# Performance work log

Measured on AMD Instinct MI355X. Metric: run time of the kernel, lower is better.

Reference implementation:

```python
import jax, jax.numpy as jnp
import numpy as np

T, N = 64, 512
DL, DA, DV = 300, 128, 128
HL, HA, HV = 256, 128, 128
MEM, DF = 256, 128
H_ATT1, H_ATT2, H_G1, H_G2, H_OUT = 512, 512, 512, 512, 256
BETA, M_MOD = 2.0, 3
ATT_IN = (HL + HA + HV) * 2      # cStar dim (windowsize=2)
G_IN = ATT_IN + MEM


def setup_inputs() -> dict:
    key = jax.random.key(0)
    ks = iter(jax.random.split(key, 48))

    def p(*shape):
        return jax.random.normal(next(ks), shape, jnp.float32) * 0.05

    inp = {}
    inp["x"] = jax.random.normal(next(ks), (T, N, DL + DA + DV), jnp.float32)
    for m, (d, h) in (("l", (DL, HL)), ("a", (DA, HA)), ("v", (DV, HV))):
        inp["Wih_" + m] = p(4 * h, d)   # torch LSTMCell weight_ih [4h, d]
        inp["Whh_" + m] = p(4 * h, h)
        inp["bih_" + m] = p(4 * h)
        inp["bhh_" + m] = p(4 * h)
    inp["att1_w1"], inp["att1_b1"] = p(H_ATT1, ATT_IN), p(H_ATT1)
    inp["att1_w2"], inp["att1_b2"] = p(ATT_IN, H_ATT1), p(ATT_IN)
    inp["att2_w1"], inp["att2_b1"] = p(H_ATT2, ATT_IN), p(H_ATT2)
    inp["att2_w2"], inp["att2_b2"] = p(MEM, H_ATT2), p(MEM)
    inp["g1_w1"], inp["g1_b1"] = p(H_G1, G_IN), p(H_G1)
    inp["g1_w2"], inp["g1_b2"] = p(MEM, H_G1), p(MEM)
    inp["g2_w1"], inp["g2_b1"] = p(H_G2, G_IN), p(H_G2)
    inp["g2_w2"], inp["g2_b2"] = p(MEM, H_G2), p(MEM)
    inp["fl_w"], inp["fl_b"] = p(DF, HL), p(DF)
    inp["fa_w"], inp["fa_b"] = p(DF, HA), p(DF)
    inp["fv_w"], inp["fv_b"] = p(DF, HV), p(DF)
    inp["o_w1"], inp["o_b1"] = p(H_OUT, DF + MEM), p(H_OUT)
    inp["o_w2"], inp["o_b2"] = p(1, H_OUT), p(1)
    return inp


def _lin(z, w, b):
    return z @ w.T + b


def _lstm_cell(xt, h, c, Wih, Whh, bih, bhh):
    # torch.nn.LSTMCell: gate order i, f, g, o
    gates = xt @ Wih.T + h @ Whh.T + bih + bhh
    i, f, g, o = jnp.split(gates, 4, axis=1)
    c2 = jax.nn.sigmoid(f) * c + jax.nn.sigmoid(i) * jnp.tanh(g)
    h2 = jax.nn.sigmoid(o) * jnp.tanh(c2)
    return h2, c2


def reference(x, Wih_l, Whh_l, bih_l, bhh_l, Wih_a, Whh_a, bih_a, bhh_a,
              Wih_v, Whh_v, bih_v, bhh_v,
              att1_w1, att1_b1, att1_w2, att1_b2,
              att2_w1, att2_b1, att2_w2, att2_b2,
              g1_w1, g1_b1, g1_w2, g1_b2, g2_w1, g2_b1, g2_w2, g2_b2,
              fl_w, fl_b, fa_w, fa_b, fv_w, fv_b,
              o_w1, o_b1, o_w2, o_b2):
    n = x.shape[1]

    def step(carry, xt):
        h_l, c_l, h_a, c_a, h_v, c_v, mem = carry
        x_l, x_a, x_v = xt[:, :DL], xt[:, DL:DL + DA], xt[:, DL + DA:]
        nh_l, nc_l = _lstm_cell(x_l, h_l, c_l, Wih_l, Whh_l, bih_l, bhh_l)
        nh_a, nc_a = _lstm_cell(x_a, h_a, c_a, Wih_a, Whh_a, bih_a, bhh_a)
        nh_v, nc_v = _lstm_cell(x_v, h_v, c_v, Wih_v, Whh_v, bih_v, bhh_v)
        # cStar = [prev cells, new cells]  -> [n, ATT_IN]
        cStar = jnp.concatenate([c_l, c_a, c_v, nc_l, nc_a, nc_v], axis=1)
        att = jax.nn.softmax(
            _lin(jax.nn.relu(_lin(cStar, att1_w1, att1_b1)), att1_w2, att1_b2),
            axis=1)
        attended = att * cStar
        cHat = jnp.tanh(
            _lin(jax.nn.relu(_lin(attended, att2_w1, att2_b1)), att2_w2, att2_b2))
        both = jnp.concatenate([attended, mem], axis=1)
        gamma1 = jax.nn.sigmoid(
            _lin(jax.nn.relu(_lin(both, g1_w1, g1_b1)), g1_w2, g1_b2))
        gamma2 = jax.nn.sigmoid(
            _lin(jax.nn.relu(_lin(both, g2_w1, g2_b1)), g2_w2, g2_b2))
        mem = gamma1 * mem + gamma2 * cHat
        return (nh_l, nc_l, nh_a, nc_a, nh_v, nc_v, mem), None

    z = lambda d: jnp.zeros((n, d), x.dtype)
    init = (z(HL), z(HL), z(HA), z(HA), z(HV), z(HV), z(MEM))
    (h_l, c_l, h_a, c_a, h_v, c_v, mem), _ = jax.lax.scan(step, init, x)

    def compute_exp(logits):
        return jnp.exp(logits - jnp.max(logits))  # global max, as in source

    p_l = compute_exp(_lin(h_l, fl_w, fl_b))
    p_a = compute_exp(_lin(h_a, fa_w, fa_b))
    p_v = compute_exp(_lin(h_v, fv_w, fv_b))
    e = BETA / (M_MOD - 1)
    lav = (p_l ** e) * jnp.log(p_l) + (p_a ** e) * jnp.log(p_a) + (p_v ** e) * jnp.log(p_v)
    last_hs = jnp.concatenate([lav, mem], axis=1)
    out = _lin(jax.nn.relu(_lin(last_hs, o_w1, o_b1)), o_w2, o_b2)
    return out.flatten()
```

## Files before the change

### kernel.cpp

```cpp
#include <hip/hip_runtime.h>
#include <string.h>

typedef __bf16 bf16_t;
typedef bf16_t bf16x8 __attribute__((ext_vector_type(8)));
typedef bf16_t bf16x4 __attribute__((ext_vector_type(4)));
typedef float  f32x4  __attribute__((ext_vector_type(4)));

#define MFMA16(a,b,c) __builtin_amdgcn_mfma_f32_16x16x32_bf16((a),(b),(c),0,0,0)

#define TSTEPS 64
#define NB     512
#define DIN    556
#define LDSK   40
#define GRIDP  256
#define GXD    33

#define HWREG_XCC_ID (20 | (0 << 6) | ((4 - 1) << 11))

#define OFF_WIHP_L 0u
#define OFF_WHH_L  327680u
#define OFF_WIHP_A 589824u
#define OFF_WHH_A  655360u
#define OFF_WIHP_V 720896u
#define OFF_WHH_V  786432u
#define OFF_ATT1W1 851968u
#define OFF_ATT1W2 1376256u
#define OFF_ATT2W1 1900544u
#define OFF_ATT2W2 2424832u
#define OFF_G1W1   2555904u
#define OFF_G1W2   3211264u
#define OFF_G2W1   3342336u
#define OFF_G2W2   3997696u
#define OFF_FLW    4128768u
#define OFF_FAW    4161536u
#define OFF_FVW    4177920u

__device__ __forceinline__ float sigmoidf_(float x) {
  return 1.0f / (1.0f + __expf(-x));
}
__device__ __forceinline__ float tanhf_(float x) {
  x = fminf(fmaxf(x, -15.0f), 15.0f);
  float e = __expf(2.0f * x);
  return (e - 1.0f) / (e + 1.0f);
}

struct PArgs {
  const float* x;
  const float* bih_l; const float* bhh_l;
  const float* bih_a; const float* bhh_a;
  const float* bih_v; const float* bhh_v;
  const float* att1_b1; const float* att1_b2;
  const float* att2_b1; const float* att2_b2;
  const float* g1_b1; const float* g1_b2;
  const float* g2_b1; const float* g2_b2;
  const float* fl_b; const float* fa_b; const float* fv_b;
  const float* o_w1; const float* o_b1; const float* o_w2; const float* o_b2;
  const float* cvt_src[17];
  unsigned cvt_dst[17];
  int cvt_K[17]; int cvt_Kpad[17]; int cvt_rows[17];
  bf16_t* POOL; bf16_t* XL; bf16_t* XA; bf16_t* XV;
  bf16_t* HB0; bf16_t* HB1; float* CBUF; float* MEMF; bf16_t* MEMBF;
  bf16_t* CSTAR; bf16_t* Z1; float* LOGB; bf16_t* ATTD; bf16_t* Z3;
  float* PL; float* MAXP; float* BSUM;
  unsigned* BAR;
  float* out;
};


__device__ __forceinline__ void gbar(unsigned* bar, unsigned k, int bid) {
  __syncthreads();
  if (threadIdx.x == 0) {
    __threadfence();
    unsigned* gc   = bar + (bid & 7) * 16;
    unsigned* root = bar + 128;
    if (__hip_atomic_fetch_add(gc, 1u, __ATOMIC_ACQ_REL, __HIP_MEMORY_SCOPE_AGENT)
        == 32u * (k + 1u) - 1u) {
      __hip_atomic_fetch_add(root, 1u, __ATOMIC_ACQ_REL, __HIP_MEMORY_SCOPE_AGENT);
    }
    while (__hip_atomic_load(root, __ATOMIC_RELAXED, __HIP_MEMORY_SCOPE_AGENT)
           < 8u * (k + 1u)) {
      __builtin_amdgcn_s_sleep(1);
    }
    __threadfence();
  }
  __syncthreads();
}

__device__ __forceinline__ void lbar(unsigned* ctr, unsigned target) {
  asm volatile("s_waitcnt vmcnt(0)" ::: "memory");
  __syncthreads();
  if (threadIdx.x == 0) {
    __hip_atomic_fetch_add(ctr, 1u, __ATOMIC_RELAXED, __HIP_MEMORY_SCOPE_AGENT);
    while (__hip_atomic_load(ctr, __ATOMIC_RELAXED, __HIP_MEMORY_SCOPE_AGENT)
           < target) {
      __builtin_amdgcn_s_sleep(1);
    }
    asm volatile("buffer_inv\n\ts_waitcnt vmcnt(0)" ::: "memory");
  }
  __syncthreads();
}

__device__ __forceinline__ void gates_body(const PArgs& p, int job, int t, char* SM) {
  bf16_t* Al = (bf16_t*)SM;
  bf16_t* Wl = (bf16_t*)(SM + 5120);
  float (*Gx)[64][GXD] = (float (*)[64][GXD])(SM + 15360);

  const int tid = threadIdx.x;
  const int m0 = (job >> 4) * 64;
  const int y  = job & 15;

  const bf16_t* hin = (t & 1) ? p.HB1 : p.HB0;
  bf16_t* hout      = (t & 1) ? p.HB0 : p.HB1;

  const bf16_t *xp, *Wih, *Whh;
  int Kx, Hm, hoff, j0, oldbase, boff;
  if (y < 8) {
    xp = p.XL + (size_t)t * NB * 320; Wih = p.POOL + OFF_WIHP_L; Whh = p.POOL + OFF_WHH_L;
    Kx = 320; Hm = 256; hoff = 0; j0 = y * 32; oldbase = 0; boff = 0;
  } else if (y < 12) {
    xp = p.XA + (size_t)t * NB * 128; Wih = p.POOL + OFF_WIHP_A; Whh = p.POOL + OFF_WHH_A;
    Kx = 128; Hm = 128; hoff = 131072; j0 = (y - 8) * 32; oldbase = 256; boff = 1024;
  } else {
    xp = p.XV + (size_t)t * NB * 128; Wih = p.POOL + OFF_WIHP_V; Whh = p.POOL + OFF_WHH_V;
    Kx = 128; Hm = 128; hoff = 196608; j0 = (y - 12) * 32; oldbase = 384; boff = 1536;
  }

  const int wave = tid >> 6, lane = tid & 63;
  const int lrow = lane & 15, quad = lane >> 4;
  const int srow = tid >> 2, schunk = (tid & 3) * 8;
  const int wrow = tid >> 1, wchunk = (tid & 1) * 16;

  f32x4 acc[4][2];
  #pragma unroll
  for (int mi = 0; mi < 4; mi++)
    #pragma unroll
    for (int ni = 0; ni < 2; ni++) acc[mi][ni] = f32x4{0.f, 0.f, 0.f, 0.f};

  const int g = wrow >> 5, jr = wrow & 31;

  for (int ph = 0; ph < 2; ph++) {
    const bf16_t* Ab; const bf16_t* Wb; int lda_, ldw_, K_;
    if (ph == 0) { Ab = xp;           lda_ = Kx; K_ = Kx; Wb = Wih; ldw_ = Kx; }
    else         { Ab = hin + hoff;   lda_ = Hm; K_ = Hm; Wb = Whh; ldw_ = Hm; }

    const bf16_t* Arow = Ab + (size_t)(m0 + srow) * lda_ + schunk;
    const bf16_t* Wrow = Wb + (size_t)(g * Hm + j0 + jr) * ldw_ + wchunk;
    bf16x8 av  = *(const bf16x8*)(Arow);
    bf16x8 wv0 = *(const bf16x8*)(Wrow);
    bf16x8 wv1 = *(const bf16x8*)(Wrow + 8);

    for (int k0 = 0; k0 < K_; k0 += 32) {
      *(bf16x8*)(Al + srow * LDSK + schunk) = av;
      *(bf16x8*)(Wl + wrow * LDSK + wchunk) = wv0;
      *(bf16x8*)(Wl + wrow * LDSK + wchunk + 8) = wv1;
      __syncthreads();
      if (k0 + 32 < K_) {
        av  = *(const bf16x8*)(Arow + k0 + 32);
        wv0 = *(const bf16x8*)(Wrow + k0 + 32);
        wv1 = *(const bf16x8*)(Wrow + k0 + 40);
      }
      bf16x8 afr[4], bfr[2];
      #pragma unroll
      for (int mi = 0; mi < 4; mi++)
        afr[mi] = *(const bf16x8*)(Al + (mi * 16 + lrow) * LDSK + quad * 8);
      #pragma unroll
      for (int ni = 0; ni < 2; ni++)
        bfr[ni] = *(const bf16x8*)(Wl + (wave * 32 + ni * 16 + lrow) * LDSK + quad * 8);
      #pragma unroll
      for (int mi = 0; mi < 4; mi++)
        #pragma unroll
        for (int ni = 0; ni < 2; ni++)
          acc[mi][ni] = MFMA16(afr[mi], bfr[ni], acc[mi][ni]);
      __syncthreads();
    }
  }

  #pragma unroll
  for (int mi = 0; mi < 4; mi++)
    #pragma unroll
    for (int ni = 0; ni < 2; ni++) {
      int col = ni * 16 + lrow;
      float bv = p.BSUM[boff + wave * Hm + j0 + col];
      #pragma unroll
      for (int r = 0; r < 4; r++) {
        Gx[wave][mi * 16 + quad * 4 + r][col] = acc[mi][ni][r] + bv;
      }
    }
  __syncthreads();

  float* cbuf = p.CBUF + hoff;
  int m = tid >> 2, jb = (tid & 3) * 8;
  #pragma unroll
  for (int i = 0; i < 8; i++) {
    int j = jb + i;
    float gi = Gx[0][m][j], gf = Gx[1][m][j], gg = Gx[2][m][j], go = Gx[3][m][j];
    size_t off = (size_t)(m0 + m) * Hm + (j0 + j);
    float c_old = cbuf[off];
    float c2 = sigmoidf_(gf) * c_old + sigmoidf_(gi) * tanhf_(gg);
    float h2 = sigmoidf_(go) * tanhf_(c2);
    cbuf[off] = c2;
    hout[hoff + off] = (bf16_t)h2;
    size_t cs = (size_t)(m0 + m) * 1024 + oldbase + (j0 + j);
    p.CSTAR[cs] = (bf16_t)c_old;
    p.CSTAR[cs + 512] = (bf16_t)c2;
  }
  __syncthreads();
}

__device__ __forceinline__ void lin_body(
    const bf16_t* __restrict__ A, int lda,
    const bf16_t* __restrict__ W, int ldw,
    const float* __restrict__ bias,
    bf16_t* Cb, float* Cf, int ldc, int K, int act,
    int m0, int n0, char* SM)
{
  bf16_t* Al = (bf16_t*)SM;
  bf16_t* Wl = (bf16_t*)(SM + 5120);
  const int tid = threadIdx.x;
  const int wave = tid >> 6, lane = tid & 63;
  const int wm = (wave >> 1) * 32, wn = (wave & 1) * 32;
  const int lrow = lane & 15, quad = lane >> 4;
  const int srow = tid >> 2, schunk = (tid & 3) * 8;

  f32x4 acc[2][2];
  #pragma unroll
  for (int mi = 0; mi < 2; mi++)
    #pragma unroll
    for (int ni = 0; ni < 2; ni++) acc[mi][ni] = f32x4{0.f, 0.f, 0.f, 0.f};

  const bf16_t* Arow = A + (size_t)(m0 + srow) * lda + schunk;
  const bf16_t* Wrow = W + (size_t)(n0 + srow) * ldw + schunk;
  bf16x8 av = *(const bf16x8*)(Arow);
  bf16x8 wv = *(const bf16x8*)(Wrow);

  for (int k0 = 0; k0 < K; k0 += 32) {
    *(bf16x8*)(Al + srow * LDSK + schunk) = av;
    *(bf16x8*)(Wl + srow * LDSK + schunk) = wv;
    __syncthreads();
    if (k0 + 32 < K) {
      av = *(const bf16x8*)(Arow + k0 + 32);
      wv = *(const bf16x8*)(Wrow + k0 + 32);
    }
    bf16x8 a0 = *(const bf16x8*)(Al + (wm + lrow) * LDSK + quad * 8);
    bf16x8 a1 = *(const bf16x8*)(Al + (wm + 16 + lrow) * LDSK + quad * 8);
    bf16x8 b0 = *(const bf16x8*)(Wl + (wn + lrow) * LDSK + quad * 8);
    bf16x8 b1 = *(const bf16x8*)(Wl + (wn + 16 + lrow) * LDSK + quad * 8);
    acc[0][0] = MFMA16(a0, b0, acc[0][0]);
    acc[0][1] = MFMA16(a0, b1, acc[0][1]);
    acc[1][0] = MFMA16(a1, b0, acc[1][0]);
    acc[1][1] = MFMA16(a1, b1, acc[1][1]);
    __syncthreads();
  }
  #pragma unroll
  for (int mi = 0; mi < 2; mi++)
    #pragma unroll
    for (int ni = 0; ni < 2; ni++) {
      int row0 = m0 + wm + mi * 16 + quad * 4;
      int col = n0 + wn + ni * 16 + lrow;
      float bv = bias[col];
      #pragma unroll
      for (int r = 0; r < 4; r++) {
        float v = acc[mi][ni][r] + bv;
        if (act == 1) v = fmaxf(v, 0.f);
        size_t off = (size_t)(row0 + r) * ldc + col;
        if (Cb) Cb[off] = (bf16_t)v;
        if (Cf) Cf[off] = v;
      }
    }
}

__device__ __forceinline__ void softmax_body(const PArgs& p, int n, char* SM) {
  float* red = (float*)SM;
  const int tid = threadIdx.x;
  float4 v = *(const float4*)(p.LOGB + (size_t)n * 1024 + tid * 4);
  float mx = fmaxf(fmaxf(v.x, v.y), fmaxf(v.z, v.w));
  red[tid] = mx; __syncthreads();
  for (int s = 128; s > 0; s >>= 1) {
    if (tid < s) red[tid] = fmaxf(red[tid], red[tid + s]);
    __syncthreads();
  }
  mx = red[0]; __syncthreads();
  float e0 = __expf(v.x - mx), e1 = __expf(v.y - mx);
  float e2 = __expf(v.z - mx), e3 = __expf(v.w - mx);
  red[tid] = e0 + e1 + e2 + e3; __syncthreads();
  for (int s = 128; s > 0; s >>= 1) {
    if (tid < s) red[tid] += red[tid + s];
    __syncthreads();
  }
  float inv = 1.0f / red[0];
  bf16x4 c4 = *(const bf16x4*)(p.CSTAR + (size_t)n * 1024 + tid * 4);
  bf16x4 o;
  o[0] = (bf16_t)(e0 * inv * (float)c4[0]);
  o[1] = (bf16_t)(e1 * inv * (float)c4[1]);
  o[2] = (bf16_t)(e2 * inv * (float)c4[2]);
  o[3] = (bf16_t)(e3 * inv * (float)c4[3]);
  *(bf16x4*)(p.ATTD + (size_t)n * 1024 + tid * 4) = o;
  __syncthreads();
}

__device__ __forceinline__ void z3_body(const PArgs& p, int job, char* SM) {
  bf16_t* Al = (bf16_t*)SM;
  bf16_t* Wl = (bf16_t*)(SM + 5120);
  const int tid = threadIdx.x;
  const int m0 = (job & 7) * 64, n0 = (job >> 3) * 64;
  const int wave = tid >> 6, lane = tid & 63;
  const int wm = (wave >> 1) * 32, wn = (wave & 1) * 32;
  const int lrow = lane & 15, quad = lane >> 4;
  const int srow = tid >> 2, schunk = (tid & 3) * 8;

  const bf16_t* W; const float* b; int K, nloc;
  if (n0 < 512)       { W = p.POOL + OFF_ATT2W1; b = p.att2_b1; K = 1024; nloc = n0; }
  else if (n0 < 1024) { W = p.POOL + OFF_G1W1;  b = p.g1_b1;  K = 1280; nloc = n0 - 512; }
  else                { W = p.POOL + OFF_G2W1;  b = p.g2_b1;  K = 1280; nloc = n0 - 1024; }

  f32x4 acc[2][2];
  #pragma unroll
  for (int mi = 0; mi < 2; mi++)
    #pragma unroll
    for (int ni = 0; ni < 2; ni++) acc[mi][ni] = f32x4{0.f, 0.f, 0.f, 0.f};

  const bf16_t* Aatt = p.ATTD + (size_t)(m0 + srow) * 1024 + schunk;
  const bf16_t* Amem = p.MEMBF + (size_t)(m0 + srow) * 256 + schunk;
  const bf16_t* Wrow = W + (size_t)(nloc + srow) * K + schunk;
  bf16x8 av = *(const bf16x8*)(Aatt);
  bf16x8 wv = *(const bf16x8*)(Wrow);

  for (int k0 = 0; k0 < K; k0 += 32) {
    *(bf16x8*)(Al + srow * LDSK + schunk) = av;
    *(bf16x8*)(Wl + srow * LDSK + schunk) = wv;
    __syncthreads();
    int kn = k0 + 32;
    if (kn < K) {
      av = (kn < 1024) ? *(const bf16x8*)(Aatt + kn)
                       : *(const bf16x8*)(Amem + (kn - 1024));
      wv = *(const bf16x8*)(Wrow + kn);
    }
    bf16x8 a0 = *(const bf16x8*)(Al + (wm + lrow) * LDSK + quad * 8);
    bf16x8 a1 = *(const bf16x8*)(Al + (wm + 16 + lrow) * LDSK + quad * 8);
    bf16x8 b0 = *(const bf16x8*)(Wl + (wn + lrow) * LDSK + quad * 8);
    bf16x8 b1 = *(const bf16x8*)(Wl + (wn + 16 + lrow) * LDSK + quad * 8);
    acc[0][0] = MFMA16(a0, b0, acc[0][0]);
    acc[0][1] = MFMA16(a0, b1, acc[0][1]);
    acc[1][0] = MFMA16(a1, b0, acc[1][0]);
    acc[1][1] = MFMA16(a1, b1, acc[1][1]);
    __syncthreads();
  }
  #pragma unroll
  for (int mi = 0; mi < 2; mi++)
    #pragma unroll
    for (int ni = 0; ni < 2; ni++) {
      int row0 = m0 + wm + mi * 16 + quad * 4;
      int cloc = wn + ni * 16 + lrow;
      float bv = b[nloc + cloc];
      #pragma unroll
      for (int r = 0; r < 4; r++) {
        float v = fmaxf(acc[mi][ni][r] + bv, 0.f);
        p.Z3[(size_t)(row0 + r) * 1536 + n0 + cloc] = (bf16_t)v;
      }
    }
}

__device__ __forceinline__ void gmem_body(const PArgs& p, int job, char* SM) {
  const int tid = threadIdx.x;
  const int m0 = (job & 7) * 64, n0 = (job >> 3) * 64;
  const int wave = tid >> 6, lane = tid & 63;
  const int wm = (wave >> 1) * 32, wn = (wave & 1) * 32;
  const int lrow = lane & 15, quad = lane >> 4;
  const int srow = tid >> 2, schunk = (tid & 3) * 8;

  const bf16_t* Ws[3] = { p.POOL + OFF_ATT2W2, p.POOL + OFF_G1W2, p.POOL + OFF_G2W2 };

  f32x4 acc[3][2][2];
  #pragma unroll
  for (int s = 0; s < 3; s++)
    #pragma unroll
    for (int mi = 0; mi < 2; mi++)
      #pragma unroll
      for (int ni = 0; ni < 2; ni++) acc[s][mi][ni] = f32x4{0.f, 0.f, 0.f, 0.f};

  const bf16_t* Arow = p.Z3 + (size_t)(m0 + srow) * 1536 + schunk;
  bf16x8 avv[3], wvv[3];
  #pragma unroll
  for (int s = 0; s < 3; s++) {
    avv[s] = *(const bf16x8*)(Arow + s * 512);
    wvv[s] = *(const bf16x8*)(Ws[s] + (size_t)(n0 + srow) * 512 + schunk);
  }

  for (int k0 = 0; k0 < 512; k0 += 32) {
    #pragma unroll
    for (int s = 0; s < 3; s++) {
      bf16_t* Az = (bf16_t*)(SM + s * 5120);
      bf16_t* Wz = (bf16_t*)(SM + 15360 + s * 5120);
      *(bf16x8*)(Az + srow * LDSK + schunk) = avv[s];
      *(bf16x8*)(Wz + srow * LDSK + schunk) = wvv[s];
    }
    __syncthreads();
    if (k0 + 32 < 512) {
      #pragma unroll
      for (int s = 0; s < 3; s++) {
// ... 47 lines not shown
  }
  red[tid] = mx; __syncthreads();
  for (int s = 128; s > 0; s >>= 1) {
    if (tid < s) red[tid] = fmaxf(red[tid], red[tid + s]);
    __syncthreads();
  }
  if (tid == 0) p.MAXP[job] = red[0];
  __syncthreads();
}

__device__ __forceinline__ void out_body(const PArgs& p, int n, char* SM) {
  float* hs  = (float*)SM;
  float* red = (float*)(SM + 1536);
  float* Ms  = (float*)(SM + 2560);
  const int tid = threadIdx.x;
  if (tid < 3) {
    float m = -3.4e38f;
    #pragma unroll
    for (int i = 0; i < 16; i++) m = fmaxf(m, p.MAXP[tid * 16 + i]);
    Ms[tid] = m;
  }
  __syncthreads();
  const float M0 = Ms[0], M1 = Ms[1], M2 = Ms[2];
  for (int idx = tid; idx < 384; idx += 256) {
    float v;
    if (idx < 128) {
      float d0 = p.PL[(size_t)n * 384 + idx] - M0;
      float d1 = p.PL[(size_t)n * 384 + 128 + idx] - M1;
      float d2 = p.PL[(size_t)n * 384 + 256 + idx] - M2;
      v = __expf(d0) * d0 + __expf(d1) * d1 + __expf(d2) * d2;
    } else {
      v = p.MEMF[(size_t)n * 256 + idx - 128];
    }
    hs[idx] = v;
  }
  __syncthreads();
  float acc = p.o_b1[tid];
  const float* wr = p.o_w1 + (size_t)tid * 384;
  #pragma unroll 4
  for (int k = 0; k < 384; k += 4) {
    float4 w = *(const float4*)(wr + k);
    acc += w.x * hs[k] + w.y * hs[k + 1] + w.z * hs[k + 2] + w.w * hs[k + 3];
  }
  red[tid] = fmaxf(acc, 0.f) * p.o_w2[tid];
  __syncthreads();
  for (int s = 128; s > 0; s >>= 1) {
    if (tid < s) red[tid] += red[tid + s];
    __syncthreads();
  }
  if (tid == 0) p.out[n] = red[0] + p.o_b2[0];
  __syncthreads();
}

__global__ void __launch_bounds__(256) persist_kernel(PArgs p) {
  __shared__ __align__(16) char SM[49152];
  __shared__ int meta[12];
  const int bid = blockIdx.x;
  const int tid = threadIdx.x;
  unsigned bk = 0;

  {
    float4* z = (float4*)p.HB0;
    for (int i = bid * 256 + tid; i < 180224; i += GRIDP * 256)
      z[i] = make_float4(0.f, 0.f, 0.f, 0.f);

    int gid = bid * 256 + tid;
    if (gid < 1024)      p.BSUM[gid] = p.bih_l[gid] + p.bhh_l[gid];
    else if (gid < 1536) p.BSUM[gid] = p.bih_a[gid - 1024] + p.bhh_a[gid - 1024];
    else if (gid < 2048) p.BSUM[gid] = p.bih_v[gid - 1536] + p.bhh_v[gid - 1536];

    for (int r = bid; r < TSTEPS * NB; r += GRIDP) {
      const float4* xr = (const float4*)(p.x + (size_t)r * DIN);
      int q = tid;
      if (q < 144) {
        float4 v; bf16_t* dst;
        if (q < 80) {
          v = (q < 75) ? xr[q] : make_float4(0.f, 0.f, 0.f, 0.f);
          dst = p.XL + (size_t)r * 320 + q * 4;
        } else if (q < 112) {
          v = xr[75 + (q - 80)];
          dst = p.XA + (size_t)r * 128 + (q - 80) * 4;
        } else {
          v = xr[107 + (q - 112)];
          dst = p.XV + (size_t)r * 128 + (q - 112) * 4;
        }
        bf16x4 o;
        o[0] = (bf16_t)v.x; o[1] = (bf16_t)v.y; o[2] = (bf16_t)v.z; o[3] = (bf16_t)v.w;
        *(bf16x4*)dst = o;
      }
    }

    for (int m = 0; m < 17; m++) {
      const float* src = p.cvt_src[m];
      bf16_t* dst = p.POOL + p.cvt_dst[m];
      int K = p.cvt_K[m], Kp = p.cvt_Kpad[m], R = p.cvt_rows[m];
      int Kq = Kp >> 2, Ksq = K >> 2;
      for (int r = bid; r < R; r += GRIDP) {
        const float4* sr = (const float4*)(src + (size_t)r * K);
        for (int q = tid; q < Kq; q += 256) {
          float4 v = (q < Ksq) ? sr[q] : make_float4(0.f, 0.f, 0.f, 0.f);
          bf16x4 o;
          o[0] = (bf16_t)v.x; o[1] = (bf16_t)v.y; o[2] = (bf16_t)v.z; o[3] = (bf16_t)v.w;
          *(bf16x4*)(dst + (size_t)r * Kp + q * 4) = o;
        }
      }
    }

    if (tid == 0) {
      unsigned raw = __builtin_amdgcn_s_getreg(HWREG_XCC_ID);
      if (raw > 7u) {
        __hip_atomic_store(p.BAR + 159, 1u, __ATOMIC_RELAXED, __HIP_MEMORY_SCOPE_AGENT);
        raw &= 7u;
      }
      meta[0] = (int)raw;
      meta[1] = (int)__hip_atomic_fetch_add(p.BAR + 160 + raw * 16, 1u,
                    __ATOMIC_RELAXED, __HIP_MEMORY_SCOPE_AGENT);
    }
  }
  gbar(p.BAR, bk++, bid);

  if (tid < 8)
    meta[2 + tid] = (int)__hip_atomic_load(p.BAR + 160 + tid * 16,
                        __ATOMIC_RELAXED, __HIP_MEMORY_SCOPE_AGENT);
  if (tid == 8)
    meta[10] = (int)__hip_atomic_load(p.BAR + 159,
                   __ATOMIC_RELAXED, __HIP_MEMORY_SCOPE_AGENT);
  __syncthreads();
  int total = 0; bool localmode = (meta[10] == 0);
  #pragma unroll
  for (int i = 0; i < 8; i++) {
    total += meta[2 + i];
    if (meta[2 + i] == 0) localmode = false;
  }
  if (total != GRIDP) localmode = false;

  if (localmode) {
    const int g = meta[0];
    const int rank = meta[1];
    const unsigned cnt = (unsigned)meta[2 + g];
    unsigned* lctr = p.BAR + 288 + g * 16;
    unsigned lk = 0;

    for (int t = 0; t < TSTEPS; t++) {
      for (int j = rank; j < 16; j += (int)cnt) gates_body(p, g * 16 + j, t, SM);
      lbar(lctr, cnt * (++lk));

      for (int j = rank; j < 8; j += (int)cnt)
        lin_body(p.CSTAR, 1024, p.POOL + OFF_ATT1W1, 1024, p.att1_b1,
                 p.Z1, (float*)0, 512, 1024, 1, g * 64, j * 64, SM);
      lbar(lctr, cnt * (++lk));

      for (int j = rank; j < 16; j += (int)cnt)
        lin_body(p.Z1, 512, p.POOL + OFF_ATT1W2, 512, p.att1_b2,
                 (bf16_t*)0, p.LOGB, 1024, 512, 0, g * 64, j * 64, SM);
      lbar(lctr, cnt * (++lk));

      for (int j = rank; j < 64; j += (int)cnt) softmax_body(p, g * 64 + j, SM);
      lbar(lctr, cnt * (++lk));

      for (int j = rank; j < 24; j += (int)cnt) z3_body(p, (j << 3) | g, SM);
      lbar(lctr, cnt * (++lk));

      for (int j = rank; j < 4; j += (int)cnt) gmem_body(p, (j << 3) | g, SM);
    }
  } else {
    for (int t = 0; t < TSTEPS; t++) {
      for (int job = bid; job < 128; job += GRIDP) gates_body(p, job, t, SM);
      gbar(p.BAR, bk++, bid);

      for (int job = bid; job < 64; job += GRIDP)
        lin_body(p.CSTAR, 1024, p.POOL + OFF_ATT1W1, 1024, p.att1_b1,
                 p.Z1, (float*)0, 512, 1024, 1, (job & 7) * 64, (job >> 3) * 64, SM);
      gbar(p.BAR, bk++, bid);

      for (int job = bid; job < 128; job += GRIDP)
        lin_body(p.Z1, 512, p.POOL + OFF_ATT1W2, 512, p.att1_b2,
                 (bf16_t*)0, p.LOGB, 1024, 512, 0, (job & 7) * 64, (job >> 3) * 64, SM);
      gbar(p.BAR, bk++, bid);

      for (int job = bid; job < 512; job += GRIDP) softmax_body(p, job, SM);
      gbar(p.BAR, bk++, bid);

      for (int job = bid; job < 192; job += GRIDP) z3_body(p, job, SM);
      gbar(p.BAR, bk++, bid);

      for (int job = bid; job < 32; job += GRIDP) gmem_body(p, job, SM);
    }
  }
  gbar(p.BAR, bk++, bid);

  for (int job = bid; job < 48; job += GRIDP) {
    int mat = job >> 4, rem = job & 15;
    int m0 = (rem & 7) * 64, n0 = (rem >> 3) * 64;
    const bf16_t* h = (mat == 0) ? p.HB0 : (mat == 1) ? p.HB0 + 131072 : p.HB0 + 196608;
    int lda = (mat == 0) ? 256 : 128;
    const bf16_t* W = p.POOL + ((mat == 0) ? OFF_FLW : (mat == 1) ? OFF_FAW : OFF_FVW);
    const float* b = (mat == 0) ? p.fl_b : (mat == 1) ? p.fa_b : p.fv_b;
    lin_body(h, lda, W, lda, b, (bf16_t*)0, p.PL + mat * 128, 384, lda, 0, m0, n0, SM);
  }
  gbar(p.BAR, bk++, bid);

  for (int job = bid; job < 48; job += GRIDP) maxpart_body(p, job, SM);
  gbar(p.BAR, bk++, bid);

  for (int job = bid; job < 512; job += GRIDP) out_body(p, job, SM);
}


__global__ __launch_bounds__(256) void zero_kernel(float4* p, int n4) {
  int i = blockIdx.x * 256 + threadIdx.x;
  if (i < n4) p[i] = make_float4(0.f, 0.f, 0.f, 0.f);
}

__global__ __launch_bounds__(256) void cvt_pad_kernel(
    const float* __restrict__ src, bf16_t* __restrict__ dst, int K, int Kpad)
{
  int r = blockIdx.x;
  for (int k = threadIdx.x; k < Kpad; k += 256)
    dst[(size_t)r * Kpad + k] = (k < K) ? (bf16_t)src[(size_t)r * K + k] : (bf16_t)0.f;
}

__global__ __launch_bounds__(256) void cvt_x_kernel(
    const float* __restrict__ x, bf16_t* __restrict__ xl,
    bf16_t* __restrict__ xa, bf16_t* __restrict__ xv)
{
  int r = blockIdx.x;
  const float* xr = x + (size_t)r * DIN;
  for (int c = threadIdx.x; c < 576; c += 256) {
    if (c < 320) {
      xl[(size_t)r * 320 + c] = (c < 300) ? (bf16_t)xr[c] : (bf16_t)0.f;
    } else if (c < 448) {
      xa[(size_t)r * 128 + (c - 320)] = (bf16_t)xr[300 + (c - 320)];
    } else {
      xv[(size_t)r * 128 + (c - 448)] = (bf16_t)xr[428 + (c - 448)];
    }
  }
}

__global__ __launch_bounds__(256) void bias_sum_kernel(
    const float* __restrict__ bih_l, const float* __restrict__ bhh_l,
    const float* __restrict__ bih_a, const float* __restrict__ bhh_a,
    const float* __restrict__ bih_v, const float* __restrict__ bhh_v,
    float* __restrict__ bsum)
{
  int i = blockIdx.x * 256 + threadIdx.x;
  if (i < 1024)      bsum[i] = bih_l[i] + bhh_l[i];
  else if (i < 1536) bsum[i] = bih_a[i - 1024] + bhh_a[i - 1024];
  else if (i < 2048) bsum[i] = bih_v[i - 1536] + bhh_v[i - 1536];
}

__global__ __launch_bounds__(256) void gates_cell_kernel_fb(PArgs p, int t) {
  __shared__ __align__(16) char SM[49152];
  gates_body(p, blockIdx.x * 16 + blockIdx.y, t, SM);
}

__global__ __launch_bounds__(256) void mfma_lin_kernel_fb(
    const bf16_t* A, int lda, const bf16_t* W, int ldw,
    const float* bias, bf16_t* Cb, float* Cf, int ldc, int K, int act)
{
  __shared__ __align__(16) char SM[10240];
  lin_body(A, lda, W, ldw, bias, Cb, Cf, ldc, K, act,
           blockIdx.x * 64, blockIdx.y * 64, SM);
}

__global__ __launch_bounds__(256) void softmax_attend_kernel_fb(PArgs p) {
  __shared__ __align__(16) char SM[1024];
  softmax_body(p, blockIdx.x, SM);
}

__global__ __launch_bounds__(256) void z3_kernel_fb(PArgs p) {
  __shared__ __align__(16) char SM[10240];
  z3_body(p, blockIdx.x + blockIdx.y * 8, SM);
}

__global__ __launch_bounds__(256) void gmem_kernel_fb(PArgs p) {
  __shared__ __align__(16) char SM[30720];
  gmem_body(p, blockIdx.x + blockIdx.y * 8, SM);
}

__global__ __launch_bounds__(256) void maxpart_kernel_fb(PArgs p) {
  __shared__ __align__(16) char SM[1024];
  maxpart_body(p, blockIdx.x, SM);
}

__global__ __launch_bounds__(256) void out_kernel_fb(PArgs p) {
  __shared__ __align__(16) char SM[2576];
  out_body(p, blockIdx.x, SM);
}

extern "C" void kernel_launch(void* const* d_in, const int* in_sizes, int n_in,
                              void* d_out, int out_size, void* d_ws, size_t ws_size,
                              hipStream_t stream)
{
  const float* x      = (const float*)d_in[0];
  const float* Wih_l  = (const float*)d_in[1];
  const float* Whh_l  = (const float*)d_in[2];
  const float* bih_l  = (const float*)d_in[3];
  const float* bhh_l  = (const float*)d_in[4];
  const float* Wih_a  = (const float*)d_in[5];
  const float* Whh_a  = (const float*)d_in[6];
  const float* bih_a  = (const float*)d_in[7];
  const float* bhh_a  = (const float*)d_in[8];
  const float* Wih_v  = (const float*)d_in[9];
  const float* Whh_v  = (const float*)d_in[10];
  const float* bih_v  = (const float*)d_in[11];
  const float* bhh_v  = (const float*)d_in[12];
  const float* att1_w1 = (const float*)d_in[13];
  const float* att1_b1 = (const float*)d_in[14];
  const float* att1_w2 = (const float*)d_in[15];
  const float* att1_b2 = (const float*)d_in[16];
  const float* att2_w1 = (const float*)d_in[17];
  const float* att2_b1 = (const float*)d_in[18];
  const float* att2_w2 = (const float*)d_in[19];
  const float* att2_b2 = (const float*)d_in[20];
  const float* g1_w1  = (const float*)d_in[21];
  const float* g1_b1  = (const float*)d_in[22];
  const float* g1_w2  = (const float*)d_in[23];
  const float* g1_b2  = (const float*)d_in[24];
  const float* g2_w1  = (const float*)d_in[25];
  const float* g2_b1  = (const float*)d_in[26];
  const float* g2_w2  = (const float*)d_in[27];
  const float* g2_b2  = (const float*)d_in[28];
  const float* fl_w   = (const float*)d_in[29];
  const float* fl_b   = (const float*)d_in[30];
  const float* fa_w   = (const float*)d_in[31];
  const float* fa_b   = (const float*)d_in[32];
  const float* fv_w   = (const float*)d_in[33];
  const float* fv_b   = (const float*)d_in[34];
  const float* o_w1   = (const float*)d_in[35];
  const float* o_b1   = (const float*)d_in[36];
  const float* o_w2   = (const float*)d_in[37];
  const float* o_b2   = (const float*)d_in[38];

  char* base = (char*)d_ws;
  PArgs pa;
  pa.x = x;
  pa.bih_l = bih_l; pa.bhh_l = bhh_l;
  pa.bih_a = bih_a; pa.bhh_a = bhh_a;
  pa.bih_v = bih_v; pa.bhh_v = bhh_v;
  pa.att1_b1 = att1_b1; pa.att1_b2 = att1_b2;
  pa.att2_b1 = att2_b1; pa.att2_b2 = att2_b2;
  pa.g1_b1 = g1_b1; pa.g1_b2 = g1_b2;
  pa.g2_b1 = g2_b1; pa.g2_b2 = g2_b2;
  pa.fl_b = fl_b; pa.fa_b = fa_b; pa.fv_b = fv_b;
  pa.o_w1 = o_w1; pa.o_b1 = o_b1; pa.o_w2 = o_w2; pa.o_b2 = o_b2;

  const float* csrc[17] = { Wih_l, Whh_l, Wih_a, Whh_a, Wih_v, Whh_v,
                            att1_w1, att1_w2, att2_w1, att2_w2,
                            g1_w1, g1_w2, g2_w1, g2_w2, fl_w, fa_w, fv_w };
  const unsigned cdst[17] = { OFF_WIHP_L, OFF_WHH_L, OFF_WIHP_A, OFF_WHH_A,
                              OFF_WIHP_V, OFF_WHH_V, OFF_ATT1W1, OFF_ATT1W2,
                              OFF_ATT2W1, OFF_ATT2W2, OFF_G1W1, OFF_G1W2,
                              OFF_G2W1, OFF_G2W2, OFF_FLW, OFF_FAW, OFF_FVW };
  const int cK[17]   = { 300, 256, 128, 128, 128, 128, 1024, 512, 1024, 512,
                         1280, 512, 1280, 512, 256, 128, 128 };
  const int cKp[17]  = { 320, 256, 128, 128, 128, 128, 1024, 512, 1024, 512,
                         1280, 512, 1280, 512, 256, 128, 128 };
  const int cR[17]   = { 1024, 1024, 512, 512, 512, 512, 512, 1024, 512, 256,
                         512, 256, 512, 256, 128, 128, 128 };
  for (int i = 0; i < 17; i++) {
    pa.cvt_src[i] = csrc[i]; pa.cvt_dst[i] = cdst[i];
    pa.cvt_K[i] = cK[i]; pa.cvt_Kpad[i] = cKp[i]; pa.cvt_rows[i] = cR[i];
  }

  pa.POOL  = (bf16_t*)(base);
  pa.XL    = (bf16_t*)(base + 8388608);
  pa.XA    = (bf16_t*)(base + 29360128);
  pa.XV    = (bf16_t*)(base + 37748736);
  pa.HB0   = (bf16_t*)(base + 46137344);
  pa.HB1   = (bf16_t*)(base + 46661632);
  pa.CBUF  = (float*) (base + 47185920);
  pa.MEMF  = (float*) (base + 48234496);
  pa.MEMBF = (bf16_t*)(base + 48758784);
  pa.CSTAR = (bf16_t*)(base + 49020928);
  pa.Z1    = (bf16_t*)(base + 50069504);
  pa.LOGB  = (float*) (base + 50593792);
  pa.ATTD  = (bf16_t*)(base + 52690944);
  pa.Z3    = (bf16_t*)(base + 53739520);
  pa.PL    = (float*) (base + 55312384);
  pa.MAXP  = (float*) (base + 56098816);
  pa.BSUM  = (float*) (base + 56099072);
  pa.BAR   = (unsigned*)(base + 56107264);
  pa.out   = (float*)d_out;

  hipMemsetAsync(pa.BAR, 0, 2048, stream);

  void* kargs[] = { (void*)&pa };
  hipError_t e = hipLaunchCooperativeKernel((const void*)persist_kernel,
                                            dim3(GRIDP), dim3(256), kargs, 0, stream);
  if (e == hipSuccess) return;

  zero_kernel<<<704, 256, 0, stream>>>((float4*)pa.HB0, 180224);
  cvt_x_kernel<<<TSTEPS * NB, 256, 0, stream>>>(x, pa.XL, pa.XA, pa.XV);
  for (int i = 0; i < 17; i++)
    cvt_pad_kernel<<<cR[i], 256, 0, stream>>>(csrc[i], pa.POOL + cdst[i], cK[i], cKp[i]);
  bias_sum_kernel<<<8, 256, 0, stream>>>(bih_l, bhh_l, bih_a, bhh_a, bih_v, bhh_v, pa.BSUM);

  for (int t = 0; t < TSTEPS; t++) {
    gates_cell_kernel_fb<<<dim3(8, 16), 256, 0, stream>>>(pa, t);
    mfma_lin_kernel_fb<<<dim3(8, 8), 256, 0, stream>>>(
        pa.CSTAR, 1024, pa.POOL + OFF_ATT1W1, 1024, att1_b1,
        pa.Z1, (float*)nullptr, 512, 1024, 1);
    mfma_lin_kernel_fb<<<dim3(8, 16), 256, 0, stream>>>(
        pa.Z1, 512, pa.POOL + OFF_ATT1W2, 512, att1_b2,
        (bf16_t*)nullptr, pa.LOGB, 1024, 512, 0);
    softmax_attend_kernel_fb<<<512, 256, 0, stream>>>(pa);
    z3_kernel_fb<<<dim3(8, 24), 256, 0, stream>>>(pa);
    gmem_kernel_fb<<<dim3(8, 4), 256, 0, stream>>>(pa);
  }

  bf16_t* h_l = pa.HB0;
  bf16_t* h_a = pa.HB0 + 131072;
  bf16_t* h_v = pa.HB0 + 196608;
  mfma_lin_kernel_fb<<<dim3(8, 2), 256, 0, stream>>>(
      h_l, 256, pa.POOL + OFF_FLW, 256, fl_b, (bf16_t*)nullptr, pa.PL, 384, 256, 0);
  mfma_lin_kernel_fb<<<dim3(8, 2), 256, 0, stream>>>(
      h_a, 128, pa.POOL + OFF_FAW, 128, fa_b, (bf16_t*)nullptr, pa.PL + 128, 384, 128, 0);
  mfma_lin_kernel_fb<<<dim3(8, 2), 256, 0, stream>>>(
      h_v, 128, pa.POOL + OFF_FVW, 128, fv_b, (bf16_t*)nullptr, pa.PL + 256, 384, 128, 0);
  maxpart_kernel_fb<<<48, 256, 0, stream>>>(pa);
  out_kernel_fb<<<512, 256, 0, stream>>>(pa);
}
```

Measured before the change: 4.829 ms.

## Overlap LSTM gates with previous step's attention chain via team split and double-buffered LDS

Splits each XCC group of 32 blocks into a team of 8 that computes LSTM gates for step t and a team of 24 that runs the attention/memory chain for step t-1. The chain reads a double-buffered cStar (CSTAR/CSTAR2), which makes this possible because the memory update does not feed back into the LSTM. All MFMA GEMM bodies also get double-buffered LDS tiles, so one barrier per k-iteration is removed. This adds a second counter barrier set, enlarges the barrier memset, requires extra workspace (gated by ws_size), and adds a missing gbar in the fallback path.

```diff
diff --git a/kernel.cpp b/kernel.cpp
--- a/kernel.cpp
+++ b/kernel.cpp
@@ -60,10 +60,11 @@
   int cvt_K[17]; int cvt_Kpad[17]; int cvt_rows[17];
   bf16_t* POOL; bf16_t* XL; bf16_t* XA; bf16_t* XV;
   bf16_t* HB0; bf16_t* HB1; float* CBUF; float* MEMF; bf16_t* MEMBF;
-  bf16_t* CSTAR; bf16_t* Z1; float* LOGB; bf16_t* ATTD; bf16_t* Z3;
+  bf16_t* CSTAR; bf16_t* CSTAR2; bf16_t* Z1; float* LOGB; bf16_t* ATTD; bf16_t* Z3;
   float* PL; float* MAXP; float* BSUM;
   unsigned* BAR;
   float* out;
+  int allow_team;
 };
 
 
@@ -100,17 +101,17 @@
   __syncthreads();
 }
 
-__device__ __forceinline__ void gates_body(const PArgs& p, int job, int t, char* SM) {
-  bf16_t* Al = (bf16_t*)SM;
-  bf16_t* Wl = (bf16_t*)(SM + 5120);
-  float (*Gx)[64][GXD] = (float (*)[64][GXD])(SM + 15360);
+__device__ __forceinline__ void gates_body(const PArgs& p, int job, int t, char* SM,
+                                           const bf16_t* hbase, bf16_t* houtb,
+                                           bf16_t* cstar)
+{
+  bf16_t* AlB[2] = { (bf16_t*)SM,            (bf16_t*)(SM + 5120) };
+  bf16_t* WlB[2] = { (bf16_t*)(SM + 10240),  (bf16_t*)(SM + 20480) };
+  float (*Gx)[64][GXD] = (float (*)[64][GXD])SM;
 
   const int tid = threadIdx.x;
   const int m0 = (job >> 4) * 64;
   const int y  = job & 15;
-
-  const bf16_t* hin = (t & 1) ? p.HB1 : p.HB0;
-  bf16_t* hout      = (t & 1) ? p.HB0 : p.HB1;
 
   const bf16_t *xp, *Wih, *Whh;
   int Kx, Hm, hoff, j0, oldbase, boff;
@@ -129,50 +130,58 @@
   const int lrow = lane & 15, quad = lane >> 4;
   const int srow = tid >> 2, schunk = (tid & 3) * 8;
   const int wrow = tid >> 1, wchunk = (tid & 1) * 16;
+  const int g = wrow >> 5, jr = wrow & 31;
 
   f32x4 acc[4][2];
   #pragma unroll
   for (int mi = 0; mi < 4; mi++)
     #pragma unroll
     for (int ni = 0; ni < 2; ni++) acc[mi][ni] = f32x4{0.f, 0.f, 0.f, 0.f};
-
-  const int g = wrow >> 5, jr = wrow & 31;
 
   for (int ph = 0; ph < 2; ph++) {
     const bf16_t* Ab; const bf16_t* Wb; int lda_, ldw_, K_;
-    if (ph == 0) { Ab = xp;           lda_ = Kx; K_ = Kx; Wb = Wih; ldw_ = Kx; }
-    else         { Ab = hin + hoff;   lda_ = Hm; K_ = Hm; Wb = Whh; ldw_ = Hm; }
+    if (ph == 0) { Ab = xp;            lda_ = Kx; K_ = Kx; Wb = Wih; ldw_ = Kx; }
+    else         { Ab = hbase + hoff;  lda_ = Hm; K_ = Hm; Wb = Whh; ldw_ = Hm; }
 
     const bf16_t* Arow = Ab + (size_t)(m0 + srow) * lda_ + schunk;
     const bf16_t* Wrow = Wb + (size_t)(g * Hm + j0 + jr) * ldw_ + wchunk;
+    const int nI = K_ >> 5;
+
     bf16x8 av  = *(const bf16x8*)(Arow);
     bf16x8 wv0 = *(const bf16x8*)(Wrow);
     bf16x8 wv1 = *(const bf16x8*)(Wrow + 8);
-
-    for (int k0 = 0; k0 < K_; k0 += 32) {
-      *(bf16x8*)(Al + srow * LDSK + schunk) = av;
-      *(bf16x8*)(Wl + wrow * LDSK + wchunk) = wv0;
-      *(bf16x8*)(Wl + wrow * LDSK + wchunk + 8) = wv1;
+    *(bf16x8*)(AlB[0] + srow * LDSK + schunk) = av;
+    *(bf16x8*)(WlB[0] + wrow * LDSK + wchunk) = wv0;
+    *(bf16x8*)(WlB[0] + wrow * LDSK + wchunk + 8) = wv1;
+
+    for (int i = 0; i < nI; i++) {
+      const int cur = i & 1;
+      const bool more = (i + 1 < nI);
+      if (more) {
+        av  = *(const bf16x8*)(Arow + (i + 1) * 32);
+        wv0 = *(const bf16x8*)(Wrow + (i + 1) * 32);
+        wv1 = *(const bf16x8*)(Wrow + (i + 1) * 32 + 8);
+      }
       __syncthreads();
-      if (k0 + 32 < K_) {
-        av  = *(const bf16x8*)(Arow + k0 + 32);
-        wv0 = *(const bf16x8*)(Wrow + k0 + 32);
-        wv1 = *(const bf16x8*)(Wrow + k0 + 40);
+      if (more) {
+        *(bf16x8*)(AlB[cur ^ 1] + srow * LDSK + schunk) = av;
+        *(bf16x8*)(WlB[cur ^ 1] + wrow * LDSK + wchunk) = wv0;
+        *(bf16x8*)(WlB[cur ^ 1] + wrow * LDSK + wchunk + 8) = wv1;
       }
       bf16x8 afr[4], bfr[2];
       #pragma unroll
       for (int mi = 0; mi < 4; mi++)
-        afr[mi] = *(const bf16x8*)(Al + (mi * 16 + lrow) * LDSK + quad * 8);
+        afr[mi] = *(const bf16x8*)(AlB[cur] + (mi * 16 + lrow) * LDSK + quad * 8);
       #pragma unroll
       for (int ni = 0; ni < 2; ni++)
-        bfr[ni] = *(const bf16x8*)(Wl + (wave * 32 + ni * 16 + lrow) * LDSK + quad * 8);
+        bfr[ni] = *(const bf16x8*)(WlB[cur] + (wave * 32 + ni * 16 + lrow) * LDSK + quad * 8);
       #pragma unroll
       for (int mi = 0; mi < 4; mi++)
         #pragma unroll
         for (int ni = 0; ni < 2; ni++)
           acc[mi][ni] = MFMA16(afr[mi], bfr[ni], acc[mi][ni]);
-      __syncthreads();
-    }
+    }
+    __syncthreads();
   }
 
   #pragma unroll
@@ -199,10 +208,10 @@
     float c2 = sigmoidf_(gf) * c_old + sigmoidf_(gi) * tanhf_(gg);
     float h2 = sigmoidf_(go) * tanhf_(c2);
     cbuf[off] = c2;
-    hout[hoff + off] = (bf16_t)h2;
+    houtb[hoff + off] = (bf16_t)h2;
     size_t cs = (size_t)(m0 + m) * 1024 + oldbase + (j0 + j);
-    p.CSTAR[cs] = (bf16_t)c_old;
-    p.CSTAR[cs + 512] = (bf16_t)c2;
+    cstar[cs] = (bf16_t)c_old;
+    cstar[cs + 512] = (bf16_t)c2;
   }
   __syncthreads();
 }
@@ -214,8 +223,8 @@
     bf16_t* Cb, float* Cf, int ldc, int K, int act,
     int m0, int n0, char* SM)
 {
-  bf16_t* Al = (bf16_t*)SM;
-  bf16_t* Wl = (bf16_t*)(SM + 5120);
+  bf16_t* AlB[2] = { (bf16_t*)SM,            (bf16_t*)(SM + 5120) };
+  bf16_t* WlB[2] = { (bf16_t*)(SM + 10240),  (bf16_t*)(SM + 15360) };
   const int tid = threadIdx.x;
   const int wave = tid >> 6, lane = tid & 63;
   const int wm = (wave >> 1) * 32, wn = (wave & 1) * 32;
@@ -230,27 +239,36 @@
 
   const bf16_t* Arow = A + (size_t)(m0 + srow) * lda + schunk;
   const bf16_t* Wrow = W + (size_t)(n0 + srow) * ldw + schunk;
+  const int nI = K >> 5;
+
   bf16x8 av = *(const bf16x8*)(Arow);
   bf16x8 wv = *(const bf16x8*)(Wrow);
-
-  for (int k0 = 0; k0 < K; k0 += 32) {
-    *(bf16x8*)(Al + srow * LDSK + schunk) = av;
-    *(bf16x8*)(Wl + srow * LDSK + schunk) = wv;
+  *(bf16x8*)(AlB[0] + srow * LDSK + schunk) = av;
+  *(bf16x8*)(WlB[0] + srow * LDSK + schunk) = wv;
+
+  for (int i = 0; i < nI; i++) {
+    const int cur = i & 1;
+    const bool more = (i + 1 < nI);
+    if (more) {
+      av = *(const bf16x8*)(Arow + (i + 1) * 32);
+      wv = *(const bf16x8*)(Wrow + (i + 1) * 32);
+    }
     __syncthreads();
-    if (k0 + 32 < K) {
-      av = *(const bf16x8*)(Arow + k0 + 32);
-      wv = *(const bf16x8*)(Wrow + k0 + 32);
-    }
-    bf16x8 a0 = *(const bf16x8*)(Al + (wm + lrow) * LDSK + quad * 8);
-    bf16x8 a1 = *(const bf16x8*)(Al + (wm + 16 + lrow) * LDSK + quad * 8);
-    bf16x8 b0 = *(const bf16x8*)(Wl + (wn + lrow) * LDSK + quad * 8);
-    bf16x8 b1 = *(const bf16x8*)(Wl + (wn + 16 + lrow) * LDSK + quad * 8);
+    if (more) {
+      *(bf16x8*)(AlB[cur ^ 1] + srow * LDSK + schunk) = av;
+      *(bf16x8*)(WlB[cur ^ 1] + srow * LDSK + schunk) = wv;
+    }
+    bf16x8 a0 = *(const bf16x8*)(AlB[cur] + (wm + lrow) * LDSK + quad * 8);
+    bf16x8 a1 = *(const bf16x8*)(AlB[cur] + (wm + 16 + lrow) * LDSK + quad * 8);
+    bf16x8 b0 = *(const bf16x8*)(WlB[cur] + (wn + lrow) * LDSK + quad * 8);
+    bf16x8 b1 = *(const bf16x8*)(WlB[cur] + (wn + 16 + lrow) * LDSK + quad * 8);
     acc[0][0] = MFMA16(a0, b0, acc[0][0]);
     acc[0][1] = MFMA16(a0, b1, acc[0][1]);
     acc[1][0] = MFMA16(a1, b0, acc[1][0]);
     acc[1][1] = MFMA16(a1, b1, acc[1][1]);
-    __syncthreads();
-  }
+  }
+  __syncthreads();
+
   #pragma unroll
   for (int mi = 0; mi < 2; mi++)
     #pragma unroll
@@ -269,7 +287,8 @@
     }
 }
 
-__device__ __forceinline__ void softmax_body(const PArgs& p, int n, char* SM) {
+__device__ __forceinline__ void softmax_body(const PArgs& p, int n, char* SM,
+                                             const bf16_t* cstar) {
   float* red = (float*)SM;
   const int tid = threadIdx.x;
   float4 v = *(const float4*)(p.LOGB + (size_t)n * 1024 + tid * 4);
@@ -288,7 +307,7 @@
     __syncthreads();
   }
   float inv = 1.0f / red[0];
-  bf16x4 c4 = *(const bf16x4*)(p.CSTAR + (size_t)n * 1024 + tid * 4);
+  bf16x4 c4 = *(const bf16x4*)(cstar + (size_t)n * 1024 + tid * 4);
   bf16x4 o;
   o[0] = (bf16_t)(e0 * inv * (float)c4[0]);
   o[1] = (bf16_t)(e1 * inv * (float)c4[1]);
@@ -299,8 +318,8 @@
 }
 
 __device__ __forceinline__ void z3_body(const PArgs& p, int job, char* SM) {
-  bf16_t* Al = (bf16_t*)SM;
-  bf16_t* Wl = (bf16_t*)(SM + 5120);
+  bf16_t* AlB[2] = { (bf16_t*)SM,            (bf16_t*)(SM + 5120) };
+  bf16_t* WlB[2] = { (bf16_t*)(SM + 10240),  (bf16_t*)(SM + 15360) };
   const int tid = threadIdx.x;
   const int m0 = (job & 7) * 64, n0 = (job >> 3) * 64;
   const int wave = tid >> 6, lane = tid & 63;
@@ -322,29 +341,38 @@
   const bf16_t* Aatt = p.ATTD + (size_t)(m0 + srow) * 1024 + schunk;
   const bf16_t* Amem = p.MEMBF + (size_t)(m0 + srow) * 256 + schunk;
   const bf16_t* Wrow = W + (size_t)(nloc + srow) * K + schunk;
+  const int nI = K >> 5;
+
   bf16x8 av = *(const bf16x8*)(Aatt);
   bf16x8 wv = *(const bf16x8*)(Wrow);
-
-  for (int k0 = 0; k0 < K; k0 += 32) {
-    *(bf16x8*)(Al + srow * LDSK + schunk) = av;
-    *(bf16x8*)(Wl + srow * LDSK + schunk) = wv;
-    __syncthreads();
-    int kn = k0 + 32;
-    if (kn < K) {
+  *(bf16x8*)(AlB[0] + srow * LDSK + schunk) = av;
+  *(bf16x8*)(WlB[0] + srow * LDSK + schunk) = wv;
+
+  for (int i = 0; i < nI; i++) {
+    const int cur = i & 1;
+    const bool more = (i + 1 < nI);
+    if (more) {
+      int kn = (i + 1) * 32;
       av = (kn < 1024) ? *(const bf16x8*)(Aatt + kn)
                        : *(const bf16x8*)(Amem + (kn - 1024));
       wv = *(const bf16x8*)(Wrow + kn);
     }
-    bf16x8 a0 = *(const bf16x8*)(Al + (wm + lrow) * LDSK + quad * 8);
-    bf16x8 a1 = *(const bf16x8*)(Al + (wm + 16 + lrow) * LDSK + quad * 8);
-    bf16x8 b0 = *(const bf16x8*)(Wl + (wn + lrow) * LDSK + quad * 8);
-    bf16x8 b1 = *(const bf16x8*)(Wl + (wn + 16 + lrow) * LDSK + quad * 8);
+    __syncthreads();
+    if (more) {
+      *(bf16x8*)(AlB[cur ^ 1] + srow * LDSK + schunk) = av;
+      *(bf16x8*)(WlB[cur ^ 1] + srow * LDSK + schunk) = wv;
+    }
+    bf16x8 a0 = *(const bf16x8*)(AlB[cur] + (wm + lrow) * LDSK + quad * 8);
+    bf16x8 a1 = *(const bf16x8*)(AlB[cur] + (wm + 16 + lrow) * LDSK + quad * 8);
+    bf16x8 b0 = *(const bf16x8*)(WlB[cur] + (wn + lrow) * LDSK + quad * 8);
+    bf16x8 b1 = *(const bf16x8*)(WlB[cur] + (wn + 16 + lrow) * LDSK + quad * 8);
     acc[0][0] = MFMA16(a0, b0, acc[0][0]);
     acc[0][1] = MFMA16(a0, b1, acc[0][1]);
     acc[1][0] = MFMA16(a1, b0, acc[1][0]);
     acc[1][1] = MFMA16(a1, b1, acc[1][1]);
-    __syncthreads();
-  }
+  }
+  __syncthreads();
+
   #pragma unroll
   for (int mi = 0; mi < 2; mi++)
     #pragma unroll
@@ -498,8 +526,27 @@
   __syncthreads();
 }
 
+__device__ __forceinline__ void attn_chain(const PArgs& p, int g, int rb,
+                                           const bf16_t* cs_prev, char* SM,
+                                           unsigned* teamc, unsigned& tk)
+{
+  if (rb < 8)
+    lin_body(cs_prev, 1024, p.POOL + OFF_ATT1W1, 1024, p.att1_b1,
+             p.Z1, (float*)0, 512, 1024, 1, g * 64, rb * 64, SM);
+  lbar(teamc, 24u * (++tk));
+  if (rb < 16)
+    lin_body(p.Z1, 512, p.POOL + OFF_ATT1W2, 512, p.att1_b2,
+             (bf16_t*)0, p.LOGB, 1024, 512, 0, g * 64, rb * 64, SM);
+  lbar(teamc, 24u * (++tk));
+  for (int j = rb; j < 64; j += 24) softmax_body(p, g * 64 + j, SM, cs_prev);
+  lbar(teamc, 24u * (++tk));
+  z3_body(p, (rb << 3) | g, SM);
+  lbar(teamc, 24u * (++tk));
+  if (rb < 4) gmem_body(p, (rb << 3) | g, SM);
+}
+
 __global__ void __launch_bounds__(256) persist_kernel(PArgs p) {
-  __shared__ __align__(16) char SM[49152];
+  __shared__ __align__(16) char SM[34816];
   __shared__ int meta[12];
   const int bid = blockIdx.x;
   const int tid = threadIdx.x;
@@ -572,46 +619,41 @@
     meta[10] = (int)__hip_atomic_load(p.BAR + 159,
                    __ATOMIC_RELAXED, __HIP_MEMORY_SCOPE_AGENT);
   __syncthreads();
-  int total = 0; bool localmode = (meta[10] == 0);
-  #pragma unroll
-  for (int i = 0; i < 8; i++) {
-    total += meta[2 + i];
-    if (meta[2 + i] == 0) localmode = false;
-  }
-  if (total != GRIDP) localmode = false;
-
-  if (localmode) {
+  bool teammode = (meta[10] == 0) && (p.allow_team != 0);
+  #pragma unroll
+  for (int i = 0; i < 8; i++)
+    if (meta[2 + i] != 32) teammode = false;
+
+  if (teammode) {
     const int g = meta[0];
     const int rank = meta[1];
-    const unsigned cnt = (unsigned)meta[2 + g];
-    unsigned* lctr = p.BAR + 288 + g * 16;
-    unsigned lk = 0;
+    unsigned* fullc = p.BAR + 288 + g * 16;
+    unsigned* teamc = p.BAR + 416 + g * 16;
+    unsigned lk = 0, tk = 0;
+    const int ra = rank - 24;
+    const int rb = rank;
 
     for (int t = 0; t < TSTEPS; t++) {
-      for (int j = rank; j < 16; j += (int)cnt) gates_body(p, g * 16 + j, t, SM);
-      lbar(lctr, cnt * (++lk));
-
-      for (int j = rank; j < 8; j += (int)cnt)
-        lin_body(p.CSTAR, 1024, p.POOL + OFF_ATT1W1, 1024, p.att1_b1,
-                 p.Z1, (float*)0, 512, 1024, 1, g * 64, j * 64, SM);
-      lbar(lctr, cnt * (++lk));
-
-      for (int j = rank; j < 16; j += (int)cnt)
-        lin_body(p.Z1, 512, p.POOL + OFF_ATT1W2, 512, p.att1_b2,
-                 (bf16_t*)0, p.LOGB, 1024, 512, 0, g * 64, j * 64, SM);
-      lbar(lctr, cnt * (++lk));
-
-      for (int j = rank; j < 64; j += (int)cnt) softmax_body(p, g * 64 + j, SM);
-      lbar(lctr, cnt * (++lk));
-
-      for (int j = rank; j < 24; j += (int)cnt) z3_body(p, (j << 3) | g, SM);
-      lbar(lctr, cnt * (++lk));
-
-      for (int j = rank; j < 4; j += (int)cnt) gmem_body(p, (j << 3) | g, SM);
-    }
+      lbar(fullc, 32u * (++lk));
+      const bf16_t* hin = (t & 1) ? p.HB1 : p.HB0;
+      bf16_t* hout      = (t & 1) ? p.HB0 : p.HB1;
+      bf16_t* cs_cur    = (t & 1) ? p.CSTAR2 : p.CSTAR;
+      const bf16_t* cs_prev = (t & 1) ? p.CSTAR : p.CSTAR2;
+      if (ra >= 0) {
+        gates_body(p, g * 16 + ra,     t, SM, hin, hout, cs_cur);
+        gates_body(p, g * 16 + 8 + ra, t, SM, hin, hout, cs_cur);
+      } else if (t > 0) {
+        attn_chain(p, g, rb, cs_prev, SM, teamc, tk);
+      }
+    }
+    lbar(fullc, 32u * (++lk));
+    if (ra < 0) attn_chain(p, g, rb, p.CSTAR2, SM, teamc, tk);
   } else {
     for (int t = 0; t < TSTEPS; t++) {
-      for (int job = bid; job < 128; job += GRIDP) gates_body(p, job, t, SM);
+      const bf16_t* hin = (t & 1) ? p.HB1 : p.HB0;
+      bf16_t* hout      = (t & 1) ? p.HB0 : p.HB1;
+      for (int job = bid; job < 128; job += GRIDP)
+        gates_body(p, job, t, SM, hin, hout, p.CSTAR);
       gbar(p.BAR, bk++, bid);
 
       for (int job = bid; job < 64; job += GRIDP)
@@ -624,13 +666,15 @@
                  (bf16_t*)0, p.LOGB, 1024, 512, 0, (job & 7) * 64, (job >> 3) * 64, SM);
       gbar(p.BAR, bk++, bid);
 
-      for (int job = bid; job < 512; job += GRIDP) softmax_body(p, job, SM);
+      for (int job = bid; job < 512; job += GRIDP)
+        softmax_body(p, job, SM, p.CSTAR);
       gbar(p.BAR, bk++, bid);
 
       for (int job = bid; job < 192; job += GRIDP) z3_body(p, job, SM);
       gbar(p.BAR, bk++, bid);
 
       for (int job = bid; job < 32; job += GRIDP) gmem_body(p, job, SM);
+      gbar(p.BAR, bk++, bid);
     }
   }
   gbar(p.BAR, bk++, bid);
@@ -696,26 +740,28 @@
 }
 
 __global__ __launch_bounds__(256) void gates_cell_kernel_fb(PArgs p, int t) {
-  __shared__ __align__(16) char SM[49152];
-  gates_body(p, blockIdx.x * 16 + blockIdx.y, t, SM);
+  __shared__ __align__(16) char SM[34816];
+  const bf16_t* hin = (t & 1) ? p.HB1 : p.HB0;
+  bf16_t* hout      = (t & 1) ? p.HB0 : p.HB1;
+  gates_body(p, blockIdx.x * 16 + blockIdx.y, t, SM, hin, hout, p.CSTAR);
 }
 
 __global__ __launch_bounds__(256) void mfma_lin_kernel_fb(
     const bf16_t* A, int lda, const bf16_t* W, int ldw,
     const float* bias, bf16_t* Cb, float* Cf, int ldc, int K, int act)
 {
-  __shared__ __align__(16) char SM[10240];
+  __shared__ __align__(16) char SM[20480];
   lin_body(A, lda, W, ldw, bias, Cb, Cf, ldc, K, act,
            blockIdx.x * 64, blockIdx.y * 64, SM);
 }
 
 __global__ __launch_bounds__(256) void softmax_attend_kernel_fb(PArgs p) {
   __shared__ __align__(16) char SM[1024];
-  softmax_body(p, blockIdx.x, SM);
+  softmax_body(p, blockIdx.x, SM, p.CSTAR);
 }
 
 __global__ __launch_bounds__(256) void z3_kernel_fb(PArgs p) {
-  __shared__ __align__(16) char SM[10240];
+  __shared__ __align__(16) char SM[20480];
   z3_body(p, blockIdx.x + blockIdx.y * 8, SM);
 }
 
@@ -809,27 +855,29 @@
     pa.cvt_K[i] = cK[i]; pa.cvt_Kpad[i] = cKp[i]; pa.cvt_rows[i] = cR[i];
   }
 
-  pa.POOL  = (bf16_t*)(base);
-  pa.XL    = (bf16_t*)(base + 8388608);
-  pa.XA    = (bf16_t*)(base + 29360128);
-  pa.XV    = (bf16_t*)(base + 37748736);
-  pa.HB0   = (bf16_t*)(base + 46137344);
-  pa.HB1   = (bf16_t*)(base + 46661632);
-  pa.CBUF  = (float*) (base + 47185920);
-  pa.MEMF  = (float*) (base + 48234496);
-  pa.MEMBF = (bf16_t*)(base + 48758784);
-  pa.CSTAR = (bf16_t*)(base + 49020928);
-  pa.Z1    = (bf16_t*)(base + 50069504);
-  pa.LOGB  = (float*) (base + 50593792);
-  pa.ATTD  = (bf16_t*)(base + 52690944);
-  pa.Z3    = (bf16_t*)(base + 53739520);
-  pa.PL    = (float*) (base + 55312384);
-  pa.MAXP  = (float*) (base + 56098816);
-  pa.BSUM  = (float*) (base + 56099072);
-  pa.BAR   = (unsigned*)(base + 56107264);
-  pa.out   = (float*)d_out;
-
-  hipMemsetAsync(pa.BAR, 0, 2048, stream);
+  pa.POOL   = (bf16_t*)(base);
+  pa.XL     = (bf16_t*)(base + 8388608);
+  pa.XA     = (bf16_t*)(base + 29360128);
+  pa.XV     = (bf16_t*)(base + 37748736);
+  pa.HB0    = (bf16_t*)(base + 46137344);
+  pa.HB1    = (bf16_t*)(base + 46661632);
+  pa.CBUF   = (float*) (base + 47185920);
+  pa.MEMF   = (float*) (base + 48234496);
+  pa.MEMBF  = (bf16_t*)(base + 48758784);
+  pa.CSTAR  = (bf16_t*)(base + 49020928);
+  pa.Z1     = (bf16_t*)(base + 50069504);
+  pa.LOGB   = (float*) (base + 50593792);
+  pa.ATTD   = (bf16_t*)(base + 52690944);
+  pa.Z3     = (bf16_t*)(base + 53739520);
+  pa.PL     = (float*) (base + 55312384);
+  pa.MAXP   = (float*) (base + 56098816);
+  pa.BSUM   = (float*) (base + 56099072);
+  pa.BAR    = (unsigned*)(base + 56107264);
+  pa.CSTAR2 = (bf16_t*)(base + 56111616);
+  pa.out    = (float*)d_out;
+  pa.allow_team = (ws_size >= 57160192u) ? 1 : 0;
+
+  hipMemsetAsync(pa.BAR, 0, 4096, stream);
 
   void* kargs[] = { (void*)&pa };
   hipError_t e = hipLaunchCooperativeKernel((const void*)persist_kernel,
```

Result: faster. 4.449 ms (-7.9%).
